# Kernel optimization log

Hardware: AMD Instinct MI355X
Metric: run time of the kernel (lower is better)

Reference implementation:

```python
import jax, jax.numpy as jnp
import numpy as np

# SOM hyperparameters (match init_kwargs)
M, N = 64, 64
NODES = M * N
FEATS = 256
BATCH = 1024
LR = 0.5
RADIUS_FACTOR = 1.1
TOTAL_ITER = 100000
SIGMA = max(M, N) * RADIUS_FACTOR


def setup_inputs() -> dict:
    key = jax.random.key(0)
    k1, k2 = jax.random.split(key)
    x = jax.random.uniform(k1, (BATCH, FEATS), dtype=jnp.float32)
    map_w = jax.random.uniform(k2, (NODES, FEATS), dtype=jnp.float32)
    return {"x": x, "map_w": map_w, "iteration": 0}


def _grid_locs():
    ii, jj = jnp.meshgrid(jnp.arange(M), jnp.arange(N), indexing='ij')
    return jnp.stack([ii.ravel(), jj.ravel()], axis=1)  # (NODES, 2) int32


def reference(x, map_w, iteration):
    B = x.shape[0]
    # ---- feedforward: squared distances (B, NODES) via GEMM expansion,
    # avoiding the (B, NODES, FEATS) broadcast the TF code materializes.
    x2 = jnp.sum(x * x, axis=1, keepdims=True)          # (B, 1)
    w2 = jnp.sum(map_w * map_w, axis=1)                  # (NODES,)
    sqd = x2 + w2[None, :] - 2.0 * (x @ map_w.T)         # (B, NODES)
    bmu_indices = jnp.argmin(sqd, axis=1)                # (B,)

    # ---- backprop: neighborhood-weighted codebook update
    locs = _grid_locs()                                  # (NODES, 2)
    bmu_locs = locs[bmu_indices]                         # (B, 2)
    # grid distance^2 between every node and each sample's BMU: (B, NODES)
    d2 = jnp.sum((locs[None, :, :] - bmu_locs[:, None, :]) ** 2, axis=2).astype(jnp.float32)

    lambda_g = TOTAL_ITER / SIGMA
    decay = jnp.exp(jnp.float32(-float(iteration) / lambda_g))
    radius = SIGMA * decay + 1e-6
    lr = LR * decay

    impact = jnp.exp(-d2 / (2.0 * radius * radius))
    in_radius = (jnp.sqrt(d2) <= radius).astype(jnp.float32)
    lr_op = impact * in_radius * lr                      # (B, NODES)

    # weight_update[n,d] = sum_b lr_op[b,n] * (x[b,d] - map_w[n,d])
    # computed without the (B, NODES, FEATS) intermediate:
    upd = (jnp.einsum('bn,bd->nd', lr_op, x) - lr_op.sum(axis=0)[:, None] * map_w) / B
    new_map = map_w + upd
    return new_map, bmu_indices
```

## Files before the change

### kernel.cpp

```cpp
#include <hip/hip_runtime.h>
#include <math.h>

#define NODES 4096
#define FEATS 256
#define BATCH 1024
#define LR_C 0.5f
#define SIGMA_C 70.4f

typedef _Float16 f16x8 __attribute__((ext_vector_type(8)));
typedef float floatx4 __attribute__((ext_vector_type(4)));

__device__ __forceinline__ void get_params(int it, float& lr, float& r2, float& i2r2) {
    float decay = __expf(-(float)it * (SIGMA_C / 100000.0f));
    float radius = SIGMA_C * decay + 1e-6f;
    lr = LR_C * decay;
    r2 = radius * radius;
    i2r2 = 1.0f / (2.0f * r2);
}

__device__ __forceinline__ unsigned fkey(float f) {
    unsigned u = __float_as_uint(f);
    return (u & 0x80000000u) ? ~u : (u | 0x80000000u);
}
__device__ __forceinline__ unsigned long long shfl_xor_u64(unsigned long long v, int mask) {
    unsigned lo = (unsigned)v, hi = (unsigned)(v >> 32);
    lo = __shfl_xor(lo, mask, 64);
    hi = __shfl_xor(hi, mask, 64);
    return ((unsigned long long)hi << 32) | lo;
}

__global__ __launch_bounds__(256) void k_prep(const float* __restrict__ Wm, const float* __restrict__ X,
                                              _Float16* __restrict__ Whi, _Float16* __restrict__ Wlo,
                                              float* __restrict__ w2,
                                              _Float16* __restrict__ Xhi, _Float16* __restrict__ Xlo,
                                              _Float16* __restrict__ XT,
                                              unsigned long long* __restrict__ gmin) {
    __shared__ _Float16 T[64][72];
    const int t = threadIdx.x;
    const int blk = blockIdx.x;
    const int wave = t >> 6, lane = t & 63;
#pragma unroll
    for (int rr = 0; rr < 2; ++rr) {
        int row = blk * 8 + wave * 2 + rr;
        float4 v = *(const float4*)&Wm[(size_t)row * FEATS + lane * 4];
        union { _Float16 h[4]; float2 f2; } uh, ul;
        uh.h[0] = (_Float16)v.x; uh.h[1] = (_Float16)v.y;
        uh.h[2] = (_Float16)v.z; uh.h[3] = (_Float16)v.w;
        ul.h[0] = (_Float16)(v.x - (float)uh.h[0]);
        ul.h[1] = (_Float16)(v.y - (float)uh.h[1]);
        ul.h[2] = (_Float16)(v.z - (float)uh.h[2]);
        ul.h[3] = (_Float16)(v.w - (float)uh.h[3]);
        *(float2*)&Whi[(size_t)row * FEATS + lane * 4] = uh.f2;
        *(float2*)&Wlo[(size_t)row * FEATS + lane * 4] = ul.f2;
        float s = v.x * v.x + v.y * v.y + v.z * v.z + v.w * v.w;
#pragma unroll
        for (int off = 32; off > 0; off >>= 1) s += __shfl_down(s, off, 64);
        if (lane == 0) w2[row] = s;
    }
    if (blk < 4) gmin[blk * 256 + t] = 0xFFFFFFFFFFFFFFFFULL;
    if (blk < 64) {
        const int b0 = (blk & 15) * 64, d0 = (blk >> 4) * 64;
        {
            const int bl = t >> 2, dq = (t & 3) * 16;
            union { _Float16 h[16]; float4 q[2]; } uh, ul;
#pragma unroll
            for (int c = 0; c < 4; ++c) {
                float4 v = *(const float4*)&X[(size_t)(b0 + bl) * FEATS + d0 + dq + c * 4];
                uh.h[c * 4 + 0] = (_Float16)v.x; uh.h[c * 4 + 1] = (_Float16)v.y;
                uh.h[c * 4 + 2] = (_Float16)v.z; uh.h[c * 4 + 3] = (_Float16)v.w;
                ul.h[c * 4 + 0] = (_Float16)(v.x - (float)uh.h[c * 4 + 0]);
                ul.h[c * 4 + 1] = (_Float16)(v.y - (float)uh.h[c * 4 + 1]);
                ul.h[c * 4 + 2] = (_Float16)(v.z - (float)uh.h[c * 4 + 2]);
                ul.h[c * 4 + 3] = (_Float16)(v.w - (float)uh.h[c * 4 + 3]);
            }
            *(float4*)&Xhi[(size_t)(b0 + bl) * FEATS + d0 + dq] = uh.q[0];
            *(float4*)&Xhi[(size_t)(b0 + bl) * FEATS + d0 + dq + 8] = uh.q[1];
            *(float4*)&Xlo[(size_t)(b0 + bl) * FEATS + d0 + dq] = ul.q[0];
            *(float4*)&Xlo[(size_t)(b0 + bl) * FEATS + d0 + dq + 8] = ul.q[1];
#pragma unroll
            for (int c = 0; c < 16; ++c) T[bl][dq + c] = uh.h[c];
        }
        __syncthreads();
        {
            const int dl = t >> 2, bq = (t & 3) * 16;
            union { _Float16 h[16]; float4 q[2]; } u;
#pragma unroll
            for (int c = 0; c < 16; ++c) u.h[c] = T[bq + c][dl];
            *(float4*)&XT[(size_t)(d0 + dl) * BATCH + b0 + bq] = u.q[0];
            *(float4*)&XT[(size_t)(d0 + dl) * BATCH + b0 + bq + 8] = u.q[1];
        }
    }
}

__global__ __launch_bounds__(256) void k_gemm1min(const _Float16* __restrict__ Xhi, const _Float16* __restrict__ Xlo,
                                                  const _Float16* __restrict__ Whi, const _Float16* __restrict__ Wlo,
                                                  const float* __restrict__ w2,
                                                  unsigned long long* __restrict__ gmin) {
    __shared__ _Float16 Ah[64][40];
    __shared__ _Float16 Al[64][40];
    __shared__ _Float16 Bh[64][40];
    __shared__ _Float16 Bl[64][40];
    __shared__ unsigned long long rowmin[64][2];
    const int n0 = blockIdx.x * 64;
    const int b0 = blockIdx.y * 64;
    const int t = threadIdx.x;
    const int wave = t >> 6, lane = t & 63;
    const int wm = wave & 1, wn = wave >> 1;
    const int lm = lane & 15, quad = lane >> 4;
    const int srow = t >> 2, skoff = (t & 3) * 8;
    floatx4 acc[2][2] = {};
    for (int k0 = 0; k0 < FEATS; k0 += 32) {
        *(float4*)&Ah[srow][skoff] = *(const float4*)&Xhi[(size_t)(b0 + srow) * FEATS + k0 + skoff];
        *(float4*)&Al[srow][skoff] = *(const float4*)&Xlo[(size_t)(b0 + srow) * FEATS + k0 + skoff];
        *(float4*)&Bh[srow][skoff] = *(const float4*)&Whi[(size_t)(n0 + srow) * FEATS + k0 + skoff];
        *(float4*)&Bl[srow][skoff] = *(const float4*)&Wlo[(size_t)(n0 + srow) * FEATS + k0 + skoff];
        __syncthreads();
        f16x8 ah[2], al[2], bh[2], bl[2];
        ah[0] = *(f16x8*)&Ah[wm * 32 + lm][quad * 8];
        ah[1] = *(f16x8*)&Ah[wm * 32 + 16 + lm][quad * 8];
        al[0] = *(f16x8*)&Al[wm * 32 + lm][quad * 8];
        al[1] = *(f16x8*)&Al[wm * 32 + 16 + lm][quad * 8];
        bh[0] = *(f16x8*)&Bh[wn * 32 + lm][quad * 8];
        bh[1] = *(f16x8*)&Bh[wn * 32 + 16 + lm][quad * 8];
        bl[0] = *(f16x8*)&Bl[wn * 32 + lm][quad * 8];
        bl[1] = *(f16x8*)&Bl[wn * 32 + 16 + lm][quad * 8];
#pragma unroll
        for (int i = 0; i < 2; ++i)
#pragma unroll
            for (int j = 0; j < 2; ++j) {
                acc[i][j] = __builtin_amdgcn_mfma_f32_16x16x32_f16(ah[i], bh[j], acc[i][j], 0, 0, 0);
                acc[i][j] = __builtin_amdgcn_mfma_f32_16x16x32_f16(ah[i], bl[j], acc[i][j], 0, 0, 0);
                acc[i][j] = __builtin_amdgcn_mfma_f32_16x16x32_f16(al[i], bh[j], acc[i][j], 0, 0, 0);
            }
        __syncthreads();
    }
    const int col0 = n0 + wn * 32 + lm, col1 = col0 + 16;
    const float w20 = w2[col0], w21 = w2[col1];
#pragma unroll
    for (int i = 0; i < 2; ++i) {
#pragma unroll
        for (int r = 0; r < 4; ++r) {
            float va = w20 - 2.0f * acc[i][0][r];
            float vb = w21 - 2.0f * acc[i][1][r];
            unsigned long long ka = ((unsigned long long)fkey(va) << 32) | (unsigned)col0;
            unsigned long long kb = ((unsigned long long)fkey(vb) << 32) | (unsigned)col1;
            unsigned long long m = ka < kb ? ka : kb;
#pragma unroll
            for (int mk = 1; mk < 16; mk <<= 1) {
                unsigned long long o = shfl_xor_u64(m, mk);
                if (o < m) m = o;
            }
            if (lm == 0) rowmin[wm * 32 + i * 16 + quad * 4 + r][wn] = m;
        }
    }
    __syncthreads();
    if (t < 64) {
        unsigned long long v = rowmin[t][0];
        if (rowmin[t][1] < v) v = rowmin[t][1];
        atomicMin(&gmin[b0 + t], v);
    }
}

__global__ __launch_bounds__(256) void k_gemm2f(const _Float16* __restrict__ XT,
                                                const unsigned long long* __restrict__ gmin,
                                                const int* __restrict__ itp,
                                                const float* __restrict__ Wm,
                                                float* __restrict__ out0, float* __restrict__ out1) {
    __shared__ _Float16 As[32][136];
    __shared__ _Float16 Bs[64][136];
    __shared__ int bmu_s[1024];
    __shared__ float Svl[32];
    const int d0 = blockIdx.x * 64;
    const int n0 = blockIdx.y * 32;
    const int t = threadIdx.x;
    const int wave = t >> 6, lane = t & 63;
    const int wm = wave & 1, wn = wave >> 1;
    const int lm = lane & 15, quad = lane >> 4;

#pragma unroll
    for (int j = 0; j < 4; ++j)
        bmu_s[t + j * 256] = (int)(gmin[t + j * 256] & 0xFFFFFFFFULL);
    float lr, r2, i2r2;
    get_params(itp[0], lr, r2, i2r2);
    if (blockIdx.x == 0 && blockIdx.y < 4)
        out1[blockIdx.y * 256 + t] = (float)(int)(gmin[blockIdx.y * 256 + t] & 0xFFFFFFFFULL);
    __syncthreads();

    const int arow = t >> 3, ac = (t & 7) * 16;
    const int nn = n0 + arow;
    const int ni = nn >> 6, nj = nn & 63;
    const int brow = t >> 2, bcoff = (t & 3) * 32;

    float ssum = 0.0f;
    floatx4 acc0 = {}, acc1 = {};
    for (int k0 = 0; k0 < BATCH; k0 += 128) {
        union { _Float16 h[16]; float4 q[2]; } u;
#pragma unroll
        for (int c = 0; c < 16; ++c) {
            int m = bmu_s[k0 + ac + c];
            int di = ni - (m >> 6); di = di < 0 ? -di : di;
            int dj = nj - (m & 63); dj = dj < 0 ? -dj : dj;
            float d2f = (float)(di * di + dj * dj);
            float val = (d2f <= r2) ? lr * __expf(-d2f * i2r2) : 0.0f;
            u.h[c] = (_Float16)val;
            ssum += val;
        }
        *(float4*)&As[arow][ac] = u.q[0];
        *(float4*)&As[arow][ac + 8] = u.q[1];
#pragma unroll
        for (int c = 0; c < 4; ++c)
            *(float4*)&Bs[brow][bcoff + c * 8] =
                *(const float4*)&XT[(size_t)(d0 + brow) * BATCH + k0 + bcoff + c * 8];
        __syncthreads();
#pragma unroll
        for (int ks = 0; ks < 128; ks += 32) {
            f16x8 a = *(f16x8*)&As[wm * 16 + lm][ks + quad * 8];
            f16x8 b0 = *(f16x8*)&Bs[wn * 32 + lm][ks + quad * 8];
            f16x8 b1 = *(f16x8*)&Bs[wn * 32 + 16 + lm][ks + quad * 8];
            acc0 = __builtin_amdgcn_mfma_f32_16x16x32_f16(a, b0, acc0, 0, 0, 0);
            acc1 = __builtin_amdgcn_mfma_f32_16x16x32_f16(a, b1, acc1, 0, 0, 0);
        }
        __syncthreads();
    }
#pragma unroll
    for (int mk = 1; mk < 8; mk <<= 1) ssum += __shfl_xor(ssum, mk, 64);
    if ((t & 7) == 0) Svl[arow] = ssum;
    __syncthreads();

    const float invB = 1.0f / (float)BATCH;
#pragma unroll
    for (int r = 0; r < 4; ++r) {
        int rowN = n0 + wm * 16 + quad * 4 + r;
        float cc = 1.0f - Svl[rowN - n0] * invB;
        int col0 = d0 + wn * 32 + lm;
        int col1 = col0 + 16;
        out0[(size_t)rowN * FEATS + col0] = Wm[(size_t)rowN * FEATS + col0] * cc + acc0[r] * invB;
        out0[(size_t)rowN * FEATS + col1] = Wm[(size_t)rowN * FEATS + col1] * cc + acc1[r] * invB;
    }
}

extern "C" void kernel_launch(void* const* d_in, const int* in_sizes, int n_in,
                              void* d_out, int out_size, void* d_ws, size_t ws_size,
                              hipStream_t stream) {
    const float* X = (const float*)d_in[0];
    const float* Wm = (const float*)d_in[1];
    const int* itp = (const int*)d_in[2];
    float* out0 = (float*)d_out;
    float* out1 = out0 + (size_t)NODES * FEATS;

    char* ws = (char*)d_ws;
    float* w2       = (float*)(ws + 0);
    _Float16* Xhi   = (_Float16*)(ws + 16384);
    _Float16* Xlo   = (_Float16*)(ws + 540672);
    _Float16* XT    = (_Float16*)(ws + 1064960);
    _Float16* Whi   = (_Float16*)(ws + 1589248);
    _Float16* Wlo   = (_Float16*)(ws + 3686400);
    unsigned long long* gmin = (unsigned long long*)(ws + 5783552);

    k_prep<<<512, 256, 0, stream>>>(Wm, X, Whi, Wlo, w2, Xhi, Xlo, XT, gmin);
    k_gemm1min<<<dim3(64, 16), 256, 0, stream>>>(Xhi, Xlo, Whi, Wlo, w2, gmin);
    k_gemm2f<<<dim3(4, 128), 256, 0, stream>>>(XT, gmin, itp, Wm, out0, out1);
}
```

Before: 92.05 us.

## Fuse three SOM kernels into one cooperative kernel with grid syncs

Merges the prep, distance-GEMM/argmin and update-GEMM kernels into a single cooperative launch of 512 blocks, separated by grid-wide barriers, with the stages' shared memory unioned. Each block now does two batch tiles in the argmin stage, so the grid shrinks from 1024 blocks to 512. The aim is to remove inter-kernel launch gaps. The cost is grid-sync overhead and the requirement that all 512 blocks be co-resident, which launch_bounds(256,2) is meant to help ensure.

```diff
diff --git a/kernel.cpp b/kernel.cpp
--- a/kernel.cpp
+++ b/kernel.cpp
@@ -1,5 +1,8 @@
 #include <hip/hip_runtime.h>
+#include <hip/hip_cooperative_groups.h>
 #include <math.h>
+
+namespace cg = cooperative_groups;
 
 #define NODES 4096
 #define FEATS 256
@@ -29,16 +32,34 @@
     return ((unsigned long long)hi << 32) | lo;
 }
 
-__global__ __launch_bounds__(256) void k_prep(const float* __restrict__ Wm, const float* __restrict__ X,
-                                              _Float16* __restrict__ Whi, _Float16* __restrict__ Wlo,
-                                              float* __restrict__ w2,
-                                              _Float16* __restrict__ Xhi, _Float16* __restrict__ Xlo,
-                                              _Float16* __restrict__ XT,
-                                              unsigned long long* __restrict__ gmin) {
-    __shared__ _Float16 T[64][72];
+struct SmemP0 { _Float16 T[64][72]; };
+struct SmemP1 {
+    _Float16 Ah[64][40], Al[64][40], Bh[64][40], Bl[64][40];
+    unsigned long long rowmin[64][2];
+};
+struct SmemP2 {
+    _Float16 As[32][136];
+    _Float16 Bs[64][136];
+    int bmu[1024];
+    float Svl[32];
+};
+
+__global__ __launch_bounds__(256, 2) void k_som_fused(
+    const float* __restrict__ X, const float* __restrict__ Wm, const int* __restrict__ itp,
+    float* __restrict__ out0, float* __restrict__ out1,
+    float* __restrict__ w2,
+    _Float16* __restrict__ Xhi, _Float16* __restrict__ Xlo, _Float16* __restrict__ XT,
+    _Float16* __restrict__ Whi, _Float16* __restrict__ Wlo,
+    unsigned long long* __restrict__ gmin) {
+    __shared__ union { SmemP0 p0; SmemP1 p1; SmemP2 p2; } sm;
+    cg::grid_group grid = cg::this_grid();
+
     const int t = threadIdx.x;
     const int blk = blockIdx.x;
     const int wave = t >> 6, lane = t & 63;
+    const int wm = wave & 1, wn = wave >> 1;
+    const int lm = lane & 15, quad = lane >> 4;
+
 #pragma unroll
     for (int rr = 0; rr < 2; ++rr) {
         int row = blk * 8 + wave * 2 + rr;
@@ -78,164 +99,148 @@
             *(float4*)&Xlo[(size_t)(b0 + bl) * FEATS + d0 + dq] = ul.q[0];
             *(float4*)&Xlo[(size_t)(b0 + bl) * FEATS + d0 + dq + 8] = ul.q[1];
 #pragma unroll
-            for (int c = 0; c < 16; ++c) T[bl][dq + c] = uh.h[c];
+            for (int c = 0; c < 16; ++c) sm.p0.T[bl][dq + c] = uh.h[c];
         }
         __syncthreads();
         {
             const int dl = t >> 2, bq = (t & 3) * 16;
             union { _Float16 h[16]; float4 q[2]; } u;
 #pragma unroll
-            for (int c = 0; c < 16; ++c) u.h[c] = T[bq + c][dl];
+            for (int c = 0; c < 16; ++c) u.h[c] = sm.p0.T[bq + c][dl];
             *(float4*)&XT[(size_t)(d0 + dl) * BATCH + b0 + bq] = u.q[0];
             *(float4*)&XT[(size_t)(d0 + dl) * BATCH + b0 + bq + 8] = u.q[1];
         }
     }
-}
-
-__global__ __launch_bounds__(256) void k_gemm1min(const _Float16* __restrict__ Xhi, const _Float16* __restrict__ Xlo,
-                                                  const _Float16* __restrict__ Whi, const _Float16* __restrict__ Wlo,
-                                                  const float* __restrict__ w2,
-                                                  unsigned long long* __restrict__ gmin) {
-    __shared__ _Float16 Ah[64][40];
-    __shared__ _Float16 Al[64][40];
-    __shared__ _Float16 Bh[64][40];
-    __shared__ _Float16 Bl[64][40];
-    __shared__ unsigned long long rowmin[64][2];
-    const int n0 = blockIdx.x * 64;
-    const int b0 = blockIdx.y * 64;
-    const int t = threadIdx.x;
-    const int wave = t >> 6, lane = t & 63;
-    const int wm = wave & 1, wn = wave >> 1;
-    const int lm = lane & 15, quad = lane >> 4;
-    const int srow = t >> 2, skoff = (t & 3) * 8;
-    floatx4 acc[2][2] = {};
-    for (int k0 = 0; k0 < FEATS; k0 += 32) {
-        *(float4*)&Ah[srow][skoff] = *(const float4*)&Xhi[(size_t)(b0 + srow) * FEATS + k0 + skoff];
-        *(float4*)&Al[srow][skoff] = *(const float4*)&Xlo[(size_t)(b0 + srow) * FEATS + k0 + skoff];
-        *(float4*)&Bh[srow][skoff] = *(const float4*)&Whi[(size_t)(n0 + srow) * FEATS + k0 + skoff];
-        *(float4*)&Bl[srow][skoff] = *(const float4*)&Wlo[(size_t)(n0 + srow) * FEATS + k0 + skoff];
+
+    grid.sync();
+
+    {
+        const int nt = blk >> 3;
+        const int n0 = nt * 64;
+        const int srow = t >> 2, skoff = (t & 3) * 8;
+        for (int half = 0; half < 2; ++half) {
+            const int b0 = (((blk & 7) << 1) | half) * 64;
+            floatx4 acc[2][2] = {};
+            for (int k0 = 0; k0 < FEATS; k0 += 32) {
+                *(float4*)&sm.p1.Ah[srow][skoff] = *(const float4*)&Xhi[(size_t)(b0 + srow) * FEATS + k0 + skoff];
+                *(float4*)&sm.p1.Al[srow][skoff] = *(const float4*)&Xlo[(size_t)(b0 + srow) * FEATS + k0 + skoff];
+                *(float4*)&sm.p1.Bh[srow][skoff] = *(const float4*)&Whi[(size_t)(n0 + srow) * FEATS + k0 + skoff];
+                *(float4*)&sm.p1.Bl[srow][skoff] = *(const float4*)&Wlo[(size_t)(n0 + srow) * FEATS + k0 + skoff];
+                __syncthreads();
+                f16x8 ah[2], al[2], bh[2], bl[2];
+                ah[0] = *(f16x8*)&sm.p1.Ah[wm * 32 + lm][quad * 8];
+                ah[1] = *(f16x8*)&sm.p1.Ah[wm * 32 + 16 + lm][quad * 8];
+                al[0] = *(f16x8*)&sm.p1.Al[wm * 32 + lm][quad * 8];
+                al[1] = *(f16x8*)&sm.p1.Al[wm * 32 + 16 + lm][quad * 8];
+                bh[0] = *(f16x8*)&sm.p1.Bh[wn * 32 + lm][quad * 8];
+                bh[1] = *(f16x8*)&sm.p1.Bh[wn * 32 + 16 + lm][quad * 8];
+                bl[0] = *(f16x8*)&sm.p1.Bl[wn * 32 + lm][quad * 8];
+                bl[1] = *(f16x8*)&sm.p1.Bl[wn * 32 + 16 + lm][quad * 8];
+#pragma unroll
+                for (int i = 0; i < 2; ++i)
+#pragma unroll
+                    for (int j = 0; j < 2; ++j) {
+                        acc[i][j] = __builtin_amdgcn_mfma_f32_16x16x32_f16(ah[i], bh[j], acc[i][j], 0, 0, 0);
+                        acc[i][j] = __builtin_amdgcn_mfma_f32_16x16x32_f16(ah[i], bl[j], acc[i][j], 0, 0, 0);
+                        acc[i][j] = __builtin_amdgcn_mfma_f32_16x16x32_f16(al[i], bh[j], acc[i][j], 0, 0, 0);
+                    }
+                __syncthreads();
+            }
+            const int col0 = n0 + wn * 32 + lm, col1 = col0 + 16;
+            const float w20 = w2[col0], w21 = w2[col1];
+#pragma unroll
+            for (int i = 0; i < 2; ++i) {
+#pragma unroll
+                for (int r = 0; r < 4; ++r) {
+                    float va = w20 - 2.0f * acc[i][0][r];
+                    float vb = w21 - 2.0f * acc[i][1][r];
+                    unsigned long long ka = ((unsigned long long)fkey(va) << 32) | (unsigned)col0;
+                    unsigned long long kb = ((unsigned long long)fkey(vb) << 32) | (unsigned)col1;
+                    unsigned long long m = ka < kb ? ka : kb;
+#pragma unroll
+                    for (int mk = 1; mk < 16; mk <<= 1) {
+                        unsigned long long o = shfl_xor_u64(m, mk);
+                        if (o < m) m = o;
+                    }
+                    if (lm == 0) sm.p1.rowmin[wm * 32 + i * 16 + quad * 4 + r][wn] = m;
+                }
+            }
+            __syncthreads();
+            if (t < 64) {
+                unsigned long long v = sm.p1.rowmin[t][0];
+                if (sm.p1.rowmin[t][1] < v) v = sm.p1.rowmin[t][1];
+                atomicMin(&gmin[b0 + t], v);
+            }
+            __syncthreads();
+        }
+    }
+
+    grid.sync();
+
+    {
+        const int d0 = (blk & 3) * 64;
+        const int n0 = (blk >> 2) * 32;
+
+#pragma unroll
+        for (int j = 0; j < 4; ++j)
+            sm.p2.bmu[t + j * 256] = (int)(gmin[t + j * 256] & 0xFFFFFFFFULL);
+        float lr, r2, i2r2;
+        get_params(itp[0], lr, r2, i2r2);
+        if ((blk & 3) == 0 && (blk >> 2) < 4)
+            out1[(blk >> 2) * 256 + t] = (float)(int)(gmin[(blk >> 2) * 256 + t] & 0xFFFFFFFFULL);
         __syncthreads();
-        f16x8 ah[2], al[2], bh[2], bl[2];
-        ah[0] = *(f16x8*)&Ah[wm * 32 + lm][quad * 8];
-        ah[1] = *(f16x8*)&Ah[wm * 32 + 16 + lm][quad * 8];
-        al[0] = *(f16x8*)&Al[wm * 32 + lm][quad * 8];
-        al[1] = *(f16x8*)&Al[wm * 32 + 16 + lm][quad * 8];
-        bh[0] = *(f16x8*)&Bh[wn * 32 + lm][quad * 8];
-        bh[1] = *(f16x8*)&Bh[wn * 32 + 16 + lm][quad * 8];
-        bl[0] = *(f16x8*)&Bl[wn * 32 + lm][quad * 8];
-        bl[1] = *(f16x8*)&Bl[wn * 32 + 16 + lm][quad * 8];
-#pragma unroll
-        for (int i = 0; i < 2; ++i)
-#pragma unroll
-            for (int j = 0; j < 2; ++j) {
-                acc[i][j] = __builtin_amdgcn_mfma_f32_16x16x32_f16(ah[i], bh[j], acc[i][j], 0, 0, 0);
-                acc[i][j] = __builtin_amdgcn_mfma_f32_16x16x32_f16(ah[i], bl[j], acc[i][j], 0, 0, 0);
-                acc[i][j] = __builtin_amdgcn_mfma_f32_16x16x32_f16(al[i], bh[j], acc[i][j], 0, 0, 0);
-            }
+
+        const int arow = t >> 3, ac = (t & 7) * 16;
+        const int nn = n0 + arow;
+        const int ni = nn >> 6, nj = nn & 63;
+        const int brow = t >> 2, bcoff = (t & 3) * 32;
+
+        float ssum = 0.0f;
+        floatx4 acc0 = {}, acc1 = {};
+        for (int k0 = 0; k0 < BATCH; k0 += 128) {
+            union { _Float16 h[16]; float4 q[2]; } u;
+#pragma unroll
+            for (int c = 0; c < 16; ++c) {
+                int m = sm.p2.bmu[k0 + ac + c];
+                int di = ni - (m >> 6); di = di < 0 ? -di : di;
+                int dj = nj - (m & 63); dj = dj < 0 ? -dj : dj;
+                float d2f = (float)(di * di + dj * dj);
+                float val = (d2f <= r2) ? lr * __expf(-d2f * i2r2) : 0.0f;
+                u.h[c] = (_Float16)val;
+                ssum += val;
+            }
+            *(float4*)&sm.p2.As[arow][ac] = u.q[0];
+            *(float4*)&sm.p2.As[arow][ac + 8] = u.q[1];
+#pragma unroll
+            for (int c = 0; c < 4; ++c)
+                *(float4*)&sm.p2.Bs[brow][bcoff + c * 8] =
+                    *(const float4*)&XT[(size_t)(d0 + brow) * BATCH + k0 + bcoff + c * 8];
+            __syncthreads();
+#pragma unroll
+            for (int ks = 0; ks < 128; ks += 32) {
+                f16x8 a = *(f16x8*)&sm.p2.As[wm * 16 + lm][ks + quad * 8];
+                f16x8 b0 = *(f16x8*)&sm.p2.Bs[wn * 32 + lm][ks + quad * 8];
+                f16x8 b1 = *(f16x8*)&sm.p2.Bs[wn * 32 + 16 + lm][ks + quad * 8];
+                acc0 = __builtin_amdgcn_mfma_f32_16x16x32_f16(a, b0, acc0, 0, 0, 0);
+                acc1 = __builtin_amdgcn_mfma_f32_16x16x32_f16(a, b1, acc1, 0, 0, 0);
+            }
+            __syncthreads();
+        }
+#pragma unroll
+        for (int mk = 1; mk < 8; mk <<= 1) ssum += __shfl_xor(ssum, mk, 64);
+        if ((t & 7) == 0) sm.p2.Svl[arow] = ssum;
         __syncthreads();
-    }
-    const int col0 = n0 + wn * 32 + lm, col1 = col0 + 16;
-    const float w20 = w2[col0], w21 = w2[col1];
-#pragma unroll
-    for (int i = 0; i < 2; ++i) {
+
+        const float invB = 1.0f / (float)BATCH;
 #pragma unroll
         for (int r = 0; r < 4; ++r) {
-            float va = w20 - 2.0f * acc[i][0][r];
-            float vb = w21 - 2.0f * acc[i][1][r];
-            unsigned long long ka = ((unsigned long long)fkey(va) << 32) | (unsigned)col0;
-            unsigned long long kb = ((unsigned long long)fkey(vb) << 32) | (unsigned)col1;
-            unsigned long long m = ka < kb ? ka : kb;
-#pragma unroll
-            for (int mk = 1; mk < 16; mk <<= 1) {
-                unsigned long long o = shfl_xor_u64(m, mk);
-                if (o < m) m = o;
-            }
-            if (lm == 0) rowmin[wm * 32 + i * 16 + quad * 4 + r][wn] = m;
-        }
-    }
-    __syncthreads();
-    if (t < 64) {
-        unsigned long long v = rowmin[t][0];
-        if (rowmin[t][1] < v) v = rowmin[t][1];
-        atomicMin(&gmin[b0 + t], v);
-    }
-}
-
-__global__ __launch_bounds__(256) void k_gemm2f(const _Float16* __restrict__ XT,
-                                                const unsigned long long* __restrict__ gmin,
-                                                const int* __restrict__ itp,
-                                                const float* __restrict__ Wm,
-                                                float* __restrict__ out0, float* __restrict__ out1) {
-    __shared__ _Float16 As[32][136];
-    __shared__ _Float16 Bs[64][136];
-    __shared__ int bmu_s[1024];
-    __shared__ float Svl[32];
-    const int d0 = blockIdx.x * 64;
-    const int n0 = blockIdx.y * 32;
-    const int t = threadIdx.x;
-    const int wave = t >> 6, lane = t & 63;
-    const int wm = wave & 1, wn = wave >> 1;
-    const int lm = lane & 15, quad = lane >> 4;
-
-#pragma unroll
-    for (int j = 0; j < 4; ++j)
-        bmu_s[t + j * 256] = (int)(gmin[t + j * 256] & 0xFFFFFFFFULL);
-    float lr, r2, i2r2;
-    get_params(itp[0], lr, r2, i2r2);
-    if (blockIdx.x == 0 && blockIdx.y < 4)
-        out1[blockIdx.y * 256 + t] = (float)(int)(gmin[blockIdx.y * 256 + t] & 0xFFFFFFFFULL);
-    __syncthreads();
-
-    const int arow = t >> 3, ac = (t & 7) * 16;
-    const int nn = n0 + arow;
-    const int ni = nn >> 6, nj = nn & 63;
-    const int brow = t >> 2, bcoff = (t & 3) * 32;
-
-    float ssum = 0.0f;
-    floatx4 acc0 = {}, acc1 = {};
-    for (int k0 = 0; k0 < BATCH; k0 += 128) {
-        union { _Float16 h[16]; float4 q[2]; } u;
-#pragma unroll
-        for (int c = 0; c < 16; ++c) {
-            int m = bmu_s[k0 + ac + c];
-            int di = ni - (m >> 6); di = di < 0 ? -di : di;
-            int dj = nj - (m & 63); dj = dj < 0 ? -dj : dj;
-            float d2f = (float)(di * di + dj * dj);
-            float val = (d2f <= r2) ? lr * __expf(-d2f * i2r2) : 0.0f;
-            u.h[c] = (_Float16)val;
-            ssum += val;
-        }
-        *(float4*)&As[arow][ac] = u.q[0];
-        *(float4*)&As[arow][ac + 8] = u.q[1];
-#pragma unroll
-        for (int c = 0; c < 4; ++c)
-            *(float4*)&Bs[brow][bcoff + c * 8] =
-                *(const float4*)&XT[(size_t)(d0 + brow) * BATCH + k0 + bcoff + c * 8];
-        __syncthreads();
-#pragma unroll
-        for (int ks = 0; ks < 128; ks += 32) {
-            f16x8 a = *(f16x8*)&As[wm * 16 + lm][ks + quad * 8];
-            f16x8 b0 = *(f16x8*)&Bs[wn * 32 + lm][ks + quad * 8];
-            f16x8 b1 = *(f16x8*)&Bs[wn * 32 + 16 + lm][ks + quad * 8];
-            acc0 = __builtin_amdgcn_mfma_f32_16x16x32_f16(a, b0, acc0, 0, 0, 0);
-            acc1 = __builtin_amdgcn_mfma_f32_16x16x32_f16(a, b1, acc1, 0, 0, 0);
-        }
-        __syncthreads();
-    }
-#pragma unroll
-    for (int mk = 1; mk < 8; mk <<= 1) ssum += __shfl_xor(ssum, mk, 64);
-    if ((t & 7) == 0) Svl[arow] = ssum;
-    __syncthreads();
-
-    const float invB = 1.0f / (float)BATCH;
-#pragma unroll
-    for (int r = 0; r < 4; ++r) {
-        int rowN = n0 + wm * 16 + quad * 4 + r;
-        float cc = 1.0f - Svl[rowN - n0] * invB;
-        int col0 = d0 + wn * 32 + lm;
-        int col1 = col0 + 16;
-        out0[(size_t)rowN * FEATS + col0] = Wm[(size_t)rowN * FEATS + col0] * cc + acc0[r] * invB;
-        out0[(size_t)rowN * FEATS + col1] = Wm[(size_t)rowN * FEATS + col1] * cc + acc1[r] * invB;
+            int rowN = n0 + wm * 16 + quad * 4 + r;
+            float cc = 1.0f - sm.p2.Svl[rowN - n0] * invB;
+            int col0 = d0 + wn * 32 + lm;
+            int col1 = col0 + 16;
+            out0[(size_t)rowN * FEATS + col0] = Wm[(size_t)rowN * FEATS + col0] * cc + acc0[r] * invB;
+            out0[(size_t)rowN * FEATS + col1] = Wm[(size_t)rowN * FEATS + col1] * cc + acc1[r] * invB;
+        }
     }
 }
 
@@ -257,7 +262,8 @@
     _Float16* Wlo   = (_Float16*)(ws + 3686400);
     unsigned long long* gmin = (unsigned long long*)(ws + 5783552);
 
-    k_prep<<<512, 256, 0, stream>>>(Wm, X, Whi, Wlo, w2, Xhi, Xlo, XT, gmin);
-    k_gemm1min<<<dim3(64, 16), 256, 0, stream>>>(Xhi, Xlo, Whi, Wlo, w2, gmin);
-    k_gemm2f<<<dim3(4, 128), 256, 0, stream>>>(XT, gmin, itp, Wm, out0, out1);
-}
+    void* args[] = {(void*)&X, (void*)&Wm, (void*)&itp, (void*)&out0, (void*)&out1,
+                    (void*)&w2, (void*)&Xhi, (void*)&Xlo, (void*)&XT,
+                    (void*)&Whi, (void*)&Wlo, (void*)&gmin};
+    hipLaunchCooperativeKernel((const void*)k_som_fused, dim3(512), dim3(256), args, 0, stream);
+}
```

Measured after the change: 230.9 us. 2.51x slower.

## Fuse fp16 hi/lo split, norm, and X transpose into GEMM1 kernel

Applied to the files above, without the earlier changes.

Removes the separate prep kernel. GEMM1 now loads fp32 X and W directly, splits them into fp16 hi/lo parts in registers, computes the W row norms on the fly, and writes the transposed X tile from shared memory. gmin is initialised with a memset instead. This saves one launch and the round trip of the fp16 intermediates through global memory. In exchange, every GEMM block repeats the conversion work and reads twice as many fp32 bytes per tile, which makes the GEMM main loop heavier.

```diff
diff --git a/kernel.cpp b/kernel.cpp
--- a/kernel.cpp
+++ b/kernel.cpp
@@ -29,78 +29,15 @@
     return ((unsigned long long)hi << 32) | lo;
 }
 
-__global__ __launch_bounds__(256) void k_prep(const float* __restrict__ Wm, const float* __restrict__ X,
-                                              _Float16* __restrict__ Whi, _Float16* __restrict__ Wlo,
-                                              float* __restrict__ w2,
-                                              _Float16* __restrict__ Xhi, _Float16* __restrict__ Xlo,
-                                              _Float16* __restrict__ XT,
-                                              unsigned long long* __restrict__ gmin) {
-    __shared__ _Float16 T[64][72];
-    const int t = threadIdx.x;
-    const int blk = blockIdx.x;
-    const int wave = t >> 6, lane = t & 63;
-#pragma unroll
-    for (int rr = 0; rr < 2; ++rr) {
-        int row = blk * 8 + wave * 2 + rr;
-        float4 v = *(const float4*)&Wm[(size_t)row * FEATS + lane * 4];
-        union { _Float16 h[4]; float2 f2; } uh, ul;
-        uh.h[0] = (_Float16)v.x; uh.h[1] = (_Float16)v.y;
-        uh.h[2] = (_Float16)v.z; uh.h[3] = (_Float16)v.w;
-        ul.h[0] = (_Float16)(v.x - (float)uh.h[0]);
-        ul.h[1] = (_Float16)(v.y - (float)uh.h[1]);
-        ul.h[2] = (_Float16)(v.z - (float)uh.h[2]);
-        ul.h[3] = (_Float16)(v.w - (float)uh.h[3]);
-        *(float2*)&Whi[(size_t)row * FEATS + lane * 4] = uh.f2;
-        *(float2*)&Wlo[(size_t)row * FEATS + lane * 4] = ul.f2;
-        float s = v.x * v.x + v.y * v.y + v.z * v.z + v.w * v.w;
-#pragma unroll
-        for (int off = 32; off > 0; off >>= 1) s += __shfl_down(s, off, 64);
-        if (lane == 0) w2[row] = s;
-    }
-    if (blk < 4) gmin[blk * 256 + t] = 0xFFFFFFFFFFFFFFFFULL;
-    if (blk < 64) {
-        const int b0 = (blk & 15) * 64, d0 = (blk >> 4) * 64;
-        {
-            const int bl = t >> 2, dq = (t & 3) * 16;
-            union { _Float16 h[16]; float4 q[2]; } uh, ul;
-#pragma unroll
-            for (int c = 0; c < 4; ++c) {
-                float4 v = *(const float4*)&X[(size_t)(b0 + bl) * FEATS + d0 + dq + c * 4];
-                uh.h[c * 4 + 0] = (_Float16)v.x; uh.h[c * 4 + 1] = (_Float16)v.y;
-                uh.h[c * 4 + 2] = (_Float16)v.z; uh.h[c * 4 + 3] = (_Float16)v.w;
-                ul.h[c * 4 + 0] = (_Float16)(v.x - (float)uh.h[c * 4 + 0]);
-                ul.h[c * 4 + 1] = (_Float16)(v.y - (float)uh.h[c * 4 + 1]);
-                ul.h[c * 4 + 2] = (_Float16)(v.z - (float)uh.h[c * 4 + 2]);
-                ul.h[c * 4 + 3] = (_Float16)(v.w - (float)uh.h[c * 4 + 3]);
-            }
-            *(float4*)&Xhi[(size_t)(b0 + bl) * FEATS + d0 + dq] = uh.q[0];
-            *(float4*)&Xhi[(size_t)(b0 + bl) * FEATS + d0 + dq + 8] = uh.q[1];
-            *(float4*)&Xlo[(size_t)(b0 + bl) * FEATS + d0 + dq] = ul.q[0];
-            *(float4*)&Xlo[(size_t)(b0 + bl) * FEATS + d0 + dq + 8] = ul.q[1];
-#pragma unroll
-            for (int c = 0; c < 16; ++c) T[bl][dq + c] = uh.h[c];
-        }
-        __syncthreads();
-        {
-            const int dl = t >> 2, bq = (t & 3) * 16;
-            union { _Float16 h[16]; float4 q[2]; } u;
-#pragma unroll
-            for (int c = 0; c < 16; ++c) u.h[c] = T[bq + c][dl];
-            *(float4*)&XT[(size_t)(d0 + dl) * BATCH + b0 + bq] = u.q[0];
-            *(float4*)&XT[(size_t)(d0 + dl) * BATCH + b0 + bq + 8] = u.q[1];
-        }
-    }
-}
-
-__global__ __launch_bounds__(256) void k_gemm1min(const _Float16* __restrict__ Xhi, const _Float16* __restrict__ Xlo,
-                                                  const _Float16* __restrict__ Whi, const _Float16* __restrict__ Wlo,
-                                                  const float* __restrict__ w2,
+__global__ __launch_bounds__(256) void k_gemm1min(const float* __restrict__ X, const float* __restrict__ Wm,
+                                                  _Float16* __restrict__ XT,
                                                   unsigned long long* __restrict__ gmin) {
     __shared__ _Float16 Ah[64][40];
     __shared__ _Float16 Al[64][40];
     __shared__ _Float16 Bh[64][40];
     __shared__ _Float16 Bl[64][40];
     __shared__ unsigned long long rowmin[64][2];
+    __shared__ float w2s[64][4];
     const int n0 = blockIdx.x * 64;
     const int b0 = blockIdx.y * 64;
     const int t = threadIdx.x;
@@ -108,12 +45,27 @@
     const int wm = wave & 1, wn = wave >> 1;
     const int lm = lane & 15, quad = lane >> 4;
     const int srow = t >> 2, skoff = (t & 3) * 8;
+    float wsq = 0.0f;
     floatx4 acc[2][2] = {};
     for (int k0 = 0; k0 < FEATS; k0 += 32) {
-        *(float4*)&Ah[srow][skoff] = *(const float4*)&Xhi[(size_t)(b0 + srow) * FEATS + k0 + skoff];
-        *(float4*)&Al[srow][skoff] = *(const float4*)&Xlo[(size_t)(b0 + srow) * FEATS + k0 + skoff];
-        *(float4*)&Bh[srow][skoff] = *(const float4*)&Whi[(size_t)(n0 + srow) * FEATS + k0 + skoff];
-        *(float4*)&Bl[srow][skoff] = *(const float4*)&Wlo[(size_t)(n0 + srow) * FEATS + k0 + skoff];
+        float xa[8], wa[8];
+        *(float4*)&xa[0] = *(const float4*)&X[(size_t)(b0 + srow) * FEATS + k0 + skoff];
+        *(float4*)&xa[4] = *(const float4*)&X[(size_t)(b0 + srow) * FEATS + k0 + skoff + 4];
+        *(float4*)&wa[0] = *(const float4*)&Wm[(size_t)(n0 + srow) * FEATS + k0 + skoff];
+        *(float4*)&wa[4] = *(const float4*)&Wm[(size_t)(n0 + srow) * FEATS + k0 + skoff + 4];
+        union { _Float16 h[8]; float4 q; } xh, xl, wh, wl;
+#pragma unroll
+        for (int i = 0; i < 8; ++i) {
+            xh.h[i] = (_Float16)xa[i];
+            xl.h[i] = (_Float16)(xa[i] - (float)xh.h[i]);
+            wh.h[i] = (_Float16)wa[i];
+            wl.h[i] = (_Float16)(wa[i] - (float)wh.h[i]);
+            wsq += wa[i] * wa[i];
+        }
+        *(float4*)&Ah[srow][skoff] = xh.q;
+        *(float4*)&Al[srow][skoff] = xl.q;
+        *(float4*)&Bh[srow][skoff] = wh.q;
+        *(float4*)&Bl[srow][skoff] = wl.q;
         __syncthreads();
         f16x8 ah[2], al[2], bh[2], bl[2];
         ah[0] = *(f16x8*)&Ah[wm * 32 + lm][quad * 8];
@@ -132,10 +84,21 @@
                 acc[i][j] = __builtin_amdgcn_mfma_f32_16x16x32_f16(ah[i], bl[j], acc[i][j], 0, 0, 0);
                 acc[i][j] = __builtin_amdgcn_mfma_f32_16x16x32_f16(al[i], bh[j], acc[i][j], 0, 0, 0);
             }
-        __syncthreads();
-    }
+        if (blockIdx.x == (k0 >> 5)) {
+            const int dcol = t >> 3, bch = (t & 7) * 8;
+            union { _Float16 h[8]; float4 q; } u;
+#pragma unroll
+            for (int j = 0; j < 8; ++j) u.h[j] = Ah[bch + j][dcol];
+            *(float4*)&XT[(size_t)(k0 + dcol) * BATCH + b0 + bch] = u.q;
+        }
+        __syncthreads();
+    }
+    w2s[srow][t & 3] = wsq;
+    __syncthreads();
     const int col0 = n0 + wn * 32 + lm, col1 = col0 + 16;
-    const float w20 = w2[col0], w21 = w2[col1];
+    const int r0 = wn * 32 + lm, r1 = r0 + 16;
+    const float w20 = w2s[r0][0] + w2s[r0][1] + w2s[r0][2] + w2s[r0][3];
+    const float w21 = w2s[r1][0] + w2s[r1][1] + w2s[r1][2] + w2s[r1][3];
 #pragma unroll
     for (int i = 0; i < 2; ++i) {
 #pragma unroll
@@ -249,15 +212,10 @@
     float* out1 = out0 + (size_t)NODES * FEATS;
 
     char* ws = (char*)d_ws;
-    float* w2       = (float*)(ws + 0);
-    _Float16* Xhi   = (_Float16*)(ws + 16384);
-    _Float16* Xlo   = (_Float16*)(ws + 540672);
-    _Float16* XT    = (_Float16*)(ws + 1064960);
-    _Float16* Whi   = (_Float16*)(ws + 1589248);
-    _Float16* Wlo   = (_Float16*)(ws + 3686400);
-    unsigned long long* gmin = (unsigned long long*)(ws + 5783552);
-
-    k_prep<<<512, 256, 0, stream>>>(Wm, X, Whi, Wlo, w2, Xhi, Xlo, XT, gmin);
-    k_gemm1min<<<dim3(64, 16), 256, 0, stream>>>(Xhi, Xlo, Whi, Wlo, w2, gmin);
+    _Float16* XT = (_Float16*)(ws + 0);
+    unsigned long long* gmin = (unsigned long long*)(ws + 524288);
+
+    hipMemsetAsync(gmin, 0xFF, 1024 * sizeof(unsigned long long), stream);
+    k_gemm1min<<<dim3(64, 16), 256, 0, stream>>>(X, Wm, XT, gmin);
     k_gemm2f<<<dim3(4, 128), 256, 0, stream>>>(XT, gmin, itp, Wm, out0, out1);
 }
```

Result: faster. 89.81 us (-2.4%).
